# Optimization experiments

Measured on AMD Instinct MI355X. Metric: run time of the kernel, lower is better.

## Reference

```python
import jax, jax.numpy as jnp
import numpy as np

A = 4   # tree arity
D = 7   # tree depth; total nodes = (A**D - 1)//(A - 1) = 5461
B = 64  # batch size
E = 128 # embedding_dim
H = 128 # encode_dim
V = 50000
N_NODES = (A**D - 1) // (A - 1)


def setup_inputs() -> dict:
    key = jax.random.key(0)
    ks = jax.random.split(key, 9)
    tokens = jax.random.randint(ks[0], (N_NODES, B), 0, V, dtype=jnp.int64)
    emb = jax.random.normal(ks[1], (V, E), dtype=jnp.float32) * 0.05
    sent_w = jax.random.normal(ks[2], (H, H), dtype=jnp.float32) * 0.05
    sent_b = jax.random.normal(ks[3], (1, H), dtype=jnp.float32) * 0.05
    ctx_w = jax.random.normal(ks[4], (H, 1), dtype=jnp.float32) * 0.05
    w_ih = jax.random.normal(ks[5], (3 * H, E), dtype=jnp.float32) * 0.05
    w_hh = jax.random.normal(ks[6], (3 * H, H), dtype=jnp.float32) * 0.05
    b_ih = jax.random.normal(ks[7], (3 * H,), dtype=jnp.float32) * 0.05
    b_hh = jax.random.normal(ks[8], (3 * H,), dtype=jnp.float32) * 0.05
    return {"tokens": tokens, "emb": emb, "sent_w": sent_w, "sent_b": sent_b,
            "ctx_w": ctx_w, "w_ih": w_ih, "w_hh": w_hh, "b_ih": b_ih, "b_hh": b_hh}


def _gru_step(x, h, w_ih, w_hh, b_ih, b_hh):
    # x: [n, B, E], h: [n, B, H] -> new hidden [n, B, H]. PyTorch gate order r,z,n.
    gi = jnp.einsum('nbe,ge->nbg', x, w_ih) + b_ih   # [n, B, 3H]
    gh = jnp.einsum('nbh,gh->nbg', h, w_hh) + b_hh
    ir, iz, in_ = jnp.split(gi, 3, axis=-1)
    hr, hz, hn_ = jnp.split(gh, 3, axis=-1)
    r = jax.nn.sigmoid(ir + hr)
    z = jax.nn.sigmoid(iz + hz)
    n = jnp.tanh(in_ + r * hn_)
    return (1.0 - z) * n + z * h


def reference(tokens, emb, sent_w, sent_b, ctx_w, w_ih, w_hh, b_ih, b_hh):
    # Bottom-up over tree levels (level-order storage): level d occupies
    # tokens[(A**d-1)//(A-1) : ... + A**d]. Each node position covers the whole batch.
    hs = None       # hiddens of the level below: [A**(d+1), B, H]
    out_max = None  # running elementwise max over all node hiddens (node_list max)
    for d in range(D - 1, -1, -1):
        n = A ** d
        off = (A ** d - 1) // (A - 1)
        tok = tokens[off:off + n]          # [n, B]
        x = emb[tok]                       # [n, B, E]
        if hs is None:
            h0 = jnp.zeros((n, B, H), dtype=emb.dtype)  # leaves: no children
        else:
            ch = hs.reshape(n, A, B, H)    # children hiddens per parent
            # attention: tanh(ch @ W + b), tanh(. @ ctx), softmax over children
            u = jnp.tanh(jnp.einsum('nabh,hk->nabk', ch, sent_w) + sent_b)
            s = jnp.tanh(jnp.einsum('nabk,k->nab', u, ctx_w[:, 0]))  # [n, A, B]
            alpha = jax.nn.softmax(s, axis=1)                        # over A children
            h0 = jnp.einsum('nabh,nab->nbh', ch, alpha)              # weighted sum
        hn = _gru_step(x, h0, w_ih, w_hh, b_ih, b_hh)                # [n, B, H]
        lvl_max = hn.max(axis=0)                                     # [B, H]
        out_max = lvl_max if out_max is None else jnp.maximum(out_max, lvl_max)
        hs = hn
    return out_max  # [B, H]
```

## Files before the change

kernel.cpp:

```cpp
#include <hip/hip_runtime.h>
#include <cstdint>
#include <cstddef>


typedef short  bf16x8 __attribute__((ext_vector_type(8)));
typedef float  f32x4  __attribute__((ext_vector_type(4)));

#define WS_ACC    0u
#define WS_WIH    1048576u
#define WS_WHH    (WS_WIH + 98304u)
#define WS_SWT    (WS_WHH + 98304u)
#define WS_EMBB   (WS_SWT + 32768u)
#define WS_HLEAF  (WS_EMBB + 12800000u)
#define WS_HA     (WS_HLEAF + 12800000u)
#define WS_HB     (WS_HA + 4194304u)

__device__ __forceinline__ float sigm(float x)   { return 1.0f / (1.0f + __expf(-x)); }
__device__ __forceinline__ float tanhf_(float x) { return 1.0f - 2.0f / (1.0f + __expf(2.0f * x)); }

__device__ __forceinline__ unsigned short f2b(float f) {
  unsigned u = __float_as_uint(f);
  u += 0x7fffu + ((u >> 16) & 1u);
  return (unsigned short)(u >> 16);
}
__device__ __forceinline__ float b2f(unsigned short s) {
  return __uint_as_float(((unsigned)s) << 16);
}

__device__ __forceinline__ unsigned fenc(float f) {
  unsigned u = __float_as_uint(f);
  return (u & 0x80000000u) ? ~u : (u | 0x80000000u);
}
__device__ __forceinline__ float fdec(unsigned e) {
  unsigned u = (e & 0x80000000u) ? (e & 0x7fffffffu) : ~e;
  return __uint_as_float(u);
}

__device__ __forceinline__ f32x4 mfma16(bf16x8 a, bf16x8 b, f32x4 c) {
  return __builtin_amdgcn_mfma_f32_16x16x32_bf16(a, b, c, 0, 0, 0);
}

__global__ __launch_bounds__(256) void decode_out(const unsigned* __restrict__ acc,
                                                  float* __restrict__ out) {
  int i = blockIdx.x * 256 + threadIdx.x;
  unsigned m = 0u;
  for (int s = 0; s < 32; ++s) m = max(m, acc[s * 8192 + i]);
  out[i] = fdec(m);
}

__global__ __launch_bounds__(256) void prep_all(const float* __restrict__ emb,
                                                const float* __restrict__ wih,
                                                const float* __restrict__ whh,
                                                const float* __restrict__ sw,
                                                unsigned short* __restrict__ embb,
                                                unsigned short* __restrict__ wihb,
                                                unsigned short* __restrict__ whhb,
                                                unsigned short* __restrict__ swtb,
                                                unsigned* __restrict__ acc) {
  size_t idx = (size_t)blockIdx.x * 256 + threadIdx.x;
  if (idx < 1600000u) {
    float4 v = *(const float4*)(emb + idx * 4);
    ushort4 o; o.x = f2b(v.x); o.y = f2b(v.y); o.z = f2b(v.z); o.w = f2b(v.w);
    *(ushort4*)(embb + idx * 4) = o;
  } else if (idx < 1714688u) {
    int i = (int)(idx - 1600000u);
    if (i < 49152)       wihb[i] = f2b(wih[i]);
    else if (i < 98304)  whhb[i - 49152] = f2b(whh[i - 49152]);
    else { int j = i - 98304; int k = j >> 7, h = j & 127; swtb[j] = f2b(sw[h * 128 + k]); }
  } else {
    acc[idx - 1714688u] = 0u;
  }
}

__global__ __launch_bounds__(512, 2) void prep_hleaf(
    const unsigned short* __restrict__ embb,
    const unsigned short* __restrict__ wih,
    const float*          __restrict__ b_ih,
    const float*          __restrict__ b_hh,
    unsigned short*       __restrict__ H)
{
  __shared__ unsigned short lds[64 * 128];
  __shared__ unsigned short hvb[64 * 128];
  const int t = threadIdx.x;
  const int base = blockIdx.x * 64;

#pragma unroll
  for (int i = 0; i < 2; ++i) {
    int g = t + 512 * i;
    int m = g >> 4, c = g & 15;
    int v = base + m; if (v > 49999) v = 49999;
    uint4 vv = *(const uint4*)(embb + (size_t)v * 128 + c * 8);
    *(uint4*)(lds + m * 128 + ((c ^ (m & 15)) << 3)) = vv;
  }

  const int w = __builtin_amdgcn_readfirstlane(t >> 6);
  const int lane = t & 63, l = lane & 15, q = lane >> 4;
  const int j = w * 16 + l;

  bf16x8 Br[4], Bz[4], Bn[4];
#pragma unroll
  for (int ks = 0; ks < 4; ++ks) {
    const int ko = ks * 32 + q * 8;
    Br[ks] = *(const bf16x8*)(wih + (size_t)j * 128 + ko);
    Bz[ks] = *(const bf16x8*)(wih + (size_t)(128 + j) * 128 + ko);
    Bn[ks] = *(const bf16x8*)(wih + (size_t)(256 + j) * 128 + ko);
  }
  const float bR = b_ih[j] + b_hh[j];
  const float bZ = b_ih[128 + j] + b_hh[128 + j];
  const float bN = b_ih[256 + j];
  const float bH = b_hh[256 + j];

  f32x4 Cr[4] = {{0,0,0,0},{0,0,0,0},{0,0,0,0},{0,0,0,0}};
  f32x4 Cz[4] = {{0,0,0,0},{0,0,0,0},{0,0,0,0},{0,0,0,0}};
  f32x4 Cn[4] = {{0,0,0,0},{0,0,0,0},{0,0,0,0},{0,0,0,0}};
  __syncthreads();

#pragma unroll
  for (int ks = 0; ks < 4; ++ks) {
    bf16x8 A[4];
#pragma unroll
    for (int mt = 0; mt < 4; ++mt) {
      int m = mt * 16 + l, c = ks * 4 + q;
      A[mt] = *(const bf16x8*)(lds + m * 128 + (((c ^ l) & 15) << 3));
    }
#pragma unroll
    for (int mt = 0; mt < 4; ++mt) {
      Cr[mt] = mfma16(A[mt], Br[ks], Cr[mt]);
      Cz[mt] = mfma16(A[mt], Bz[ks], Cz[mt]);
      Cn[mt] = mfma16(A[mt], Bn[ks], Cn[mt]);
    }
  }

#pragma unroll
  for (int mt = 0; mt < 4; ++mt)
#pragma unroll
    for (int e = 0; e < 4; ++e) {
      int b = mt * 16 + q * 4 + e;
      float r  = sigm(Cr[mt][e] + bR);
      float z  = sigm(Cz[mt][e] + bZ);
      float nv = tanhf_(Cn[mt][e] + bN + r * bH);
      float hv = (1.0f - z) * nv;
      hvb[b * 128 + (j ^ (q << 4))] = f2b(hv);
    }
  __syncthreads();

#pragma unroll
  for (int i = 0; i < 2; ++i) {
    int g = t + 512 * i;
    int b = g >> 4, c8 = (g & 15) * 8;
    int qq = (b >> 2) & 3;
    if (base + b < 50000) {
      uint4 v = *(const uint4*)(hvb + b * 128 + (c8 ^ (qq << 4)));
      *(uint4*)(H + (size_t)(base + b) * 128 + c8) = v;
    }
  }
}

template <bool LEAF>
__global__ __launch_bounds__(512, 4) void attn_gru(
    const unsigned short* __restrict__ hch,
    const int*            __restrict__ tokc,
    const unsigned short* __restrict__ hleaf,
    const unsigned short* __restrict__ swt,
    const float*          __restrict__ sb,
    const float*          __restrict__ ctx,
    const int*            __restrict__ tok,
    const unsigned short* __restrict__ embb,
    const unsigned short* __restrict__ wih,
    const unsigned short* __restrict__ whh,
    const float*          __restrict__ b_ih,
    const float*          __restrict__ b_hh,
    unsigned short*       __restrict__ hout,
    unsigned*             __restrict__ acc)
{
  __shared__ unsigned short chs[128 * 128];
  __shared__ float spart[4][128];
  __shared__ float alf[128];
  unsigned short* const atile = chs;
  unsigned short* const hvb   = chs + 8192;

  const int p2 = blockIdx.x;
  const int p = p2 >> 1, half = p2 & 1;
  const int t = threadIdx.x;

  const int sm = t >> 4, sc = t & 15;
  const int* tp = tok + p * 64 + half * 32;
  uint4 px = *(const uint4*)(embb + (size_t)tp[sm] * 128 + sc * 8);

  if constexpr (LEAF) {
    const int* tokp = tokc + p * 256;
#pragma unroll
    for (int i = 0; i < 4; ++i) {
      int g = t + 512 * i, m = g >> 4, c = g & 15;
      int bg = (m >> 5) * 64 + half * 32 + (m & 31);
      uint4 v = *(const uint4*)(hleaf + (size_t)tokp[bg] * 128 + c * 8);
      *(uint4*)(chs + m * 128 + ((c ^ (m & 15)) << 3)) = v;
    }
  } else {
#pragma unroll
    for (int i = 0; i < 4; ++i) {
      int g = t + 512 * i, m = g >> 4, c = g & 15;
      int bg = (m >> 5) * 64 + half * 32 + (m & 31);
      uint4 v = *(const uint4*)(hch + ((size_t)p * 256 + bg) * 128 + c * 8);
      *(uint4*)(chs + m * 128 + ((c ^ (m & 15)) << 3)) = v;
    }
  }

  const int w = __builtin_amdgcn_readfirstlane(t >> 6);
  const int wm = w >> 2, wn = w & 3;
  const int lane = t & 63, l = lane & 15, q = lane >> 4;
  const int j = w * 16 + l;

  bf16x8 Bs[2][4];
#pragma unroll
  for (int nt = 0; nt < 2; ++nt)
#pragma unroll
    for (int ks = 0; ks < 4; ++ks)
      Bs[nt][ks] = *(const bf16x8*)(swt + (size_t)(wn * 32 + nt * 16 + l) * 128 + ks * 32 + q * 8);

  f32x4 Cu[4][2] = {};
  __syncthreads();

#pragma unroll
  for (int ks = 0; ks < 4; ++ks) {
#pragma unroll
    for (int mt = 0; mt < 4; ++mt) {
      int m = wm * 64 + mt * 16 + l;
      int c = ks * 4 + q;
      bf16x8 A = *(const bf16x8*)(chs + m * 128 + (((c ^ (m & 15)) & 15) << 3));
      Cu[mt][0] = mfma16(A, Bs[0][ks], Cu[mt][0]);
      Cu[mt][1] = mfma16(A, Bs[1][ks], Cu[mt][1]);
    }
  }

  const float sb0 = sb[wn * 32 + l],  sb1 = sb[wn * 32 + 16 + l];
  const float cx0 = ctx[wn * 32 + l], cx1 = ctx[wn * 32 + 16 + l];
#pragma unroll
  for (int mt = 0; mt < 4; ++mt) {
    float pe[4];
#pragma unroll
    for (int e = 0; e < 4; ++e)
      pe[e] = tanhf_(Cu[mt][0][e] + sb0) * cx0 + tanhf_(Cu[mt][1][e] + sb1) * cx1;
#pragma unroll
    for (int mask = 1; mask < 16; mask <<= 1)
#pragma unroll
      for (int e = 0; e < 4; ++e)
        pe[e] += __shfl_xor(pe[e], mask, 16);
    if (l == 0) {
      int r = wm * 64 + mt * 16 + q * 4;
#pragma unroll
      for (int e = 0; e < 4; ++e) spart[wn][r + e] = pe[e];
    }
  }
  __syncthreads();

  if (t < 32) {
    float sv[4];
#pragma unroll
    for (int a = 0; a < 4; ++a) {
      int r = a * 32 + t;
      sv[a] = tanhf_(spart[0][r] + spart[1][r] + spart[2][r] + spart[3][r]);
    }
    float m = fmaxf(fmaxf(sv[0], sv[1]), fmaxf(sv[2], sv[3]));
    float e0 = __expf(sv[0] - m), e1 = __expf(sv[1] - m);
    float e2 = __expf(sv[2] - m), e3 = __expf(sv[3] - m);
    float inv = 1.0f / (e0 + e1 + e2 + e3);
    alf[t] = e0 * inv; alf[32 + t] = e1 * inv; alf[64 + t] = e2 * inv; alf[96 + t] = e3 * inv;
  }
  __syncthreads();

  float o[8] = {0, 0, 0, 0, 0, 0, 0, 0};
  {
    int rb = t >> 4, c = t & 15;
#pragma unroll
    for (int a = 0; a < 4; ++a) {
      int m = a * 32 + rb;
      const unsigned short* rp = chs + m * 128 + ((c ^ (m & 15)) << 3);
      float al = alf[m];
#pragma unroll
      for (int k = 0; k < 8; ++k) o[k] += al * b2f(rp[k]);
    }
  }

  float mxv[8];
  if constexpr (LEAF) {
    const int jj = t & 127, cc = jj >> 3;
#pragma unroll
    for (int e = 0; e < 8; ++e) mxv[e] = -1e30f;
#pragma unroll
    for (int a = 0; a < 4; ++a)
#pragma unroll
      for (int e = 0; e < 8; ++e) {
        int rb = (t >> 7) + 4 * e, m = a * 32 + rb;
        float v = b2f(chs[m * 128 + (((cc ^ (m & 15)) & 15) << 3) + (jj & 7)]);
        mxv[e] = fmaxf(mxv[e], v);
      }
  }
  __syncthreads();

  *(uint4*)(atile + sm * 256 + ((sc ^ (sm & 15)) << 3)) = px;
  {
    int rb = t >> 4, c = t & 15;
    ushort4 ha, hb;
    ha.x = f2b(o[0]); ha.y = f2b(o[1]); ha.z = f2b(o[2]); ha.w = f2b(o[3]);
    hb.x = f2b(o[4]); hb.y = f2b(o[5]); hb.z = f2b(o[6]); hb.w = f2b(o[7]);
    unsigned short* dst = atile + rb * 256 + ((16 | ((c ^ (rb & 15)) & 15)) << 3);
    *(ushort4*)dst = ha;
    *(ushort4*)(dst + 4) = hb;
  }

  const unsigned short* wI = wih + (size_t)j * 128 + q * 8;
  const unsigned short* wH = whh + (size_t)j * 128 + q * 8;
  const float bR = b_ih[j] + b_hh[j];
  const float bZ = b_ih[128 + j] + b_hh[128 + j];
  const float bN = b_ih[256 + j];
  const float bH = b_hh[256 + j];
  __syncthreads();

  f32x4 Cr[2] = {{0,0,0,0},{0,0,0,0}};
  f32x4 Cz[2] = {{0,0,0,0},{0,0,0,0}};
  f32x4 Cn[2] = {{0,0,0,0},{0,0,0,0}};
  f32x4 Ch[2] = {{0,0,0,0},{0,0,0,0}};

  bf16x8 b0 = *(const bf16x8*)(wI);
  bf16x8 b1 = *(const bf16x8*)(wI + 128 * 128);
  bf16x8 b2 = *(const bf16x8*)(wI + 256 * 128);

#pragma unroll
  for (int ks = 0; ks < 8; ++ks) {
    bf16x8 c0 = b0, c1 = b1, c2 = b2;
    if (ks + 1 < 8) {
      const unsigned short* base = (ks + 1 >= 4) ? wH : wI;
      const int ko = ((ks + 1) & 3) * 32;
      b0 = *(const bf16x8*)(base + ko);
      b1 = *(const bf16x8*)(base + 128 * 128 + ko);
      b2 = *(const bf16x8*)(base + 256 * 128 + ko);
    }
#pragma unroll
    for (int mt = 0; mt < 2; ++mt) {
      int m = mt * 16 + l;
      int c = ks * 4 + q;
      bf16x8 Amt = *(const bf16x8*)(atile + m * 256 + (((c & 16) | ((c ^ l) & 15)) << 3));
      Cr[mt] = mfma16(Amt, c0, Cr[mt]);
      Cz[mt] = mfma16(Amt, c1, Cz[mt]);
      if (ks < 4) Cn[mt] = mfma16(Amt, c2, Cn[mt]);
      else        Ch[mt] = mfma16(Amt, c2, Ch[mt]);
    }
  }

  float mx[2][4];
#pragma unroll
  for (int mt = 0; mt < 2; ++mt) {
#pragma unroll
    for (int e = 0; e < 4; ++e) {
      const int b = mt * 16 + q * 4 + e;
      float r  = sigm(Cr[mt][e] + bR);
      float z  = sigm(Cz[mt][e] + bZ);
      float nv = tanhf_(Cn[mt][e] + bN + r * (Ch[mt][e] + bH));
      int c16 = j >> 3;
      float hp = b2f(atile[b * 256 + ((16 | ((c16 ^ (b & 15)) & 15)) << 3) + (j & 7)]);
      float hv = (1.0f - z) * nv + z * hp;
      hvb[b * 128 + (j ^ (q << 4))] = f2b(hv);
      mx[mt][e] = hv;
    }
  }
  __syncthreads();

  {
    int qq = (sm >> 2) & 3;
    uint4 v = *(const uint4*)(hvb + sm * 128 + ((sc * 8) ^ (qq << 4)));
    *(uint4*)(hout + ((size_t)p * 64 + half * 32 + sm) * 128 + sc * 8) = v;
  }

  unsigned* accs = acc + (p2 & 31) * 8192;
#pragma unroll
  for (int mt = 0; mt < 2; ++mt)
#pragma unroll
    for (int e = 0; e < 4; ++e) {
      const int bg = half * 32 + mt * 16 + q * 4 + e;
      atomicMax(accs + bg * 128 + j, fenc(mx[mt][e]));
    }
  if constexpr (LEAF) {
#pragma unroll
    for (int e = 0; e < 8; ++e)
      atomicMax(accs + half * 4096 + t + 512 * e, fenc(mxv[e]));
  }
}

extern "C" void kernel_launch(void* const* d_in, const int* in_sizes, int n_in,
                              void* d_out, int out_size, void* d_ws, size_t ws_size,
                              hipStream_t stream) {
  const int*   tokens = (const int*)d_in[0];
  const float* emb    = (const float*)d_in[1];
  const float* sent_w = (const float*)d_in[2];
  const float* sent_b = (const float*)d_in[3];
  const float* ctx_w  = (const float*)d_in[4];
  const float* w_ih   = (const float*)d_in[5];
  const float* w_hh   = (const float*)d_in[6];
  const float* b_ih   = (const float*)d_in[7];
  const float* b_hh   = (const float*)d_in[8];

  char* ws = (char*)d_ws;
  unsigned*       acc  = (unsigned*)(ws + WS_ACC);
  unsigned short* wihb = (unsigned short*)(ws + WS_WIH);
  unsigned short* whhb = (unsigned short*)(ws + WS_WHH);
  unsigned short* swtb = (unsigned short*)(ws + WS_SWT);
  unsigned short* embb = (unsigned short*)(ws + WS_EMBB);
  unsigned short* hlf  = (unsigned short*)(ws + WS_HLEAF);
  unsigned short* hA   = (unsigned short*)(ws + WS_HA);
  unsigned short* hB   = (unsigned short*)(ws + WS_HB);

  hipLaunchKernelGGL(prep_all, dim3(7722), dim3(256), 0, stream,
                     emb, w_ih, w_hh, sent_w, embb, wihb, whhb, swtb, acc);
  hipLaunchKernelGGL(prep_hleaf, dim3(782), dim3(512), 0, stream,
                     embb, wihb, b_ih, b_hh, hlf);

  static const int offs[7] = {0, 1, 5, 21, 85, 341, 1365};
  const int* tok6 = tokens + (size_t)1365 * 64;

  for (int d = 5; d >= 0; --d) {
    int n = 1 << (2 * d);
    unsigned short* hout  = (d & 1) ? hB : hA;
    unsigned short* child = (d & 1) ? hA : hB;
    if (d == 5) {
      hipLaunchKernelGGL((attn_gru<true>), dim3(2 * n), dim3(512), 0, stream,
                         (const unsigned short*)nullptr, tok6, hlf,
                         swtb, sent_b, ctx_w,
                         tokens + (size_t)offs[5] * 64, embb, wihb, whhb,
                         b_ih, b_hh, hout, acc);
    } else {
      hipLaunchKernelGGL((attn_gru<false>), dim3(2 * n), dim3(512), 0, stream,
                         child, (const int*)nullptr, (const unsigned short*)nullptr,
                         swtb, sent_b, ctx_w,
                         tokens + (size_t)offs[d] * 64, embb, wihb, whhb,
                         b_ih, b_hh, hout, acc);
    }
  }
  hipLaunchKernelGGL(decode_out, dim3(32), dim3(256), 0, stream, acc, (float*)d_out);
}
```

Baseline: 309.4 us.

## Make attn_gru persistent over multiple parents with register prefetch of next tile

Result: slower. 475.5 us (+53.7%).

```diff
diff --git a/kernel.cpp b/kernel.cpp
--- a/kernel.cpp
+++ b/kernel.cpp
@@ -171,40 +171,23 @@
     const float*          __restrict__ b_ih,
     const float*          __restrict__ b_hh,
     unsigned short*       __restrict__ hout,
-    unsigned*             __restrict__ acc)
+    unsigned*             __restrict__ acc,
+    int nPar, int npp)
 {
   __shared__ unsigned short chs[128 * 128];
+  __shared__ unsigned short hvb[32 * 128];
   __shared__ float spart[4][128];
   __shared__ float alf[128];
   unsigned short* const atile = chs;
-  unsigned short* const hvb   = chs + 8192;
-
-  const int p2 = blockIdx.x;
-  const int p = p2 >> 1, half = p2 & 1;
+
+  const int G = gridDim.x >> 1;
+  const int half = (blockIdx.x >= G) ? 1 : 0;
+  const int pBeg = (blockIdx.x - (half ? G : 0)) * npp;
+  const int pEnd = min(nPar, pBeg + npp);
+  if (pBeg >= nPar) return;
+
   const int t = threadIdx.x;
-
   const int sm = t >> 4, sc = t & 15;
-  const int* tp = tok + p * 64 + half * 32;
-  uint4 px = *(const uint4*)(embb + (size_t)tp[sm] * 128 + sc * 8);
-
-  if constexpr (LEAF) {
-    const int* tokp = tokc + p * 256;
-#pragma unroll
-    for (int i = 0; i < 4; ++i) {
-      int g = t + 512 * i, m = g >> 4, c = g & 15;
-      int bg = (m >> 5) * 64 + half * 32 + (m & 31);
-      uint4 v = *(const uint4*)(hleaf + (size_t)tokp[bg] * 128 + c * 8);
-      *(uint4*)(chs + m * 128 + ((c ^ (m & 15)) << 3)) = v;
-    }
-  } else {
-#pragma unroll
-    for (int i = 0; i < 4; ++i) {
-      int g = t + 512 * i, m = g >> 4, c = g & 15;
-      int bg = (m >> 5) * 64 + half * 32 + (m & 31);
-      uint4 v = *(const uint4*)(hch + ((size_t)p * 256 + bg) * 128 + c * 8);
-      *(uint4*)(chs + m * 128 + ((c ^ (m & 15)) << 3)) = v;
-    }
-  }
 
   const int w = __builtin_amdgcn_readfirstlane(t >> 6);
   const int wm = w >> 2, wn = w & 3;
@@ -218,96 +201,8 @@
     for (int ks = 0; ks < 4; ++ks)
       Bs[nt][ks] = *(const bf16x8*)(swt + (size_t)(wn * 32 + nt * 16 + l) * 128 + ks * 32 + q * 8);
 
-  f32x4 Cu[4][2] = {};
-  __syncthreads();
-
-#pragma unroll
-  for (int ks = 0; ks < 4; ++ks) {
-#pragma unroll
-    for (int mt = 0; mt < 4; ++mt) {
-      int m = wm * 64 + mt * 16 + l;
-      int c = ks * 4 + q;
-      bf16x8 A = *(const bf16x8*)(chs + m * 128 + (((c ^ (m & 15)) & 15) << 3));
-      Cu[mt][0] = mfma16(A, Bs[0][ks], Cu[mt][0]);
-      Cu[mt][1] = mfma16(A, Bs[1][ks], Cu[mt][1]);
-    }
-  }
-
   const float sb0 = sb[wn * 32 + l],  sb1 = sb[wn * 32 + 16 + l];
   const float cx0 = ctx[wn * 32 + l], cx1 = ctx[wn * 32 + 16 + l];
-#pragma unroll
-  for (int mt = 0; mt < 4; ++mt) {
-    float pe[4];
-#pragma unroll
-    for (int e = 0; e < 4; ++e)
-      pe[e] = tanhf_(Cu[mt][0][e] + sb0) * cx0 + tanhf_(Cu[mt][1][e] + sb1) * cx1;
-#pragma unroll
-    for (int mask = 1; mask < 16; mask <<= 1)
-#pragma unroll
-      for (int e = 0; e < 4; ++e)
-        pe[e] += __shfl_xor(pe[e], mask, 16);
-    if (l == 0) {
-      int r = wm * 64 + mt * 16 + q * 4;
-#pragma unroll
-      for (int e = 0; e < 4; ++e) spart[wn][r + e] = pe[e];
-    }
-  }
-  __syncthreads();
-
-  if (t < 32) {
-    float sv[4];
-#pragma unroll
-    for (int a = 0; a < 4; ++a) {
-      int r = a * 32 + t;
-      sv[a] = tanhf_(spart[0][r] + spart[1][r] + spart[2][r] + spart[3][r]);
-    }
-    float m = fmaxf(fmaxf(sv[0], sv[1]), fmaxf(sv[2], sv[3]));
-    float e0 = __expf(sv[0] - m), e1 = __expf(sv[1] - m);
-    float e2 = __expf(sv[2] - m), e3 = __expf(sv[3] - m);
-    float inv = 1.0f / (e0 + e1 + e2 + e3);
-    alf[t] = e0 * inv; alf[32 + t] = e1 * inv; alf[64 + t] = e2 * inv; alf[96 + t] = e3 * inv;
-  }
-  __syncthreads();
-
-  float o[8] = {0, 0, 0, 0, 0, 0, 0, 0};
-  {
-    int rb = t >> 4, c = t & 15;
-#pragma unroll
-    for (int a = 0; a < 4; ++a) {
-      int m = a * 32 + rb;
-      const unsigned short* rp = chs + m * 128 + ((c ^ (m & 15)) << 3);
-      float al = alf[m];
-#pragma unroll
-      for (int k = 0; k < 8; ++k) o[k] += al * b2f(rp[k]);
-    }
-  }
-
-  float mxv[8];
-  if constexpr (LEAF) {
-    const int jj = t & 127, cc = jj >> 3;
-#pragma unroll
-    for (int e = 0; e < 8; ++e) mxv[e] = -1e30f;
-#pragma unroll
-    for (int a = 0; a < 4; ++a)
-#pragma unroll
-      for (int e = 0; e < 8; ++e) {
-        int rb = (t >> 7) + 4 * e, m = a * 32 + rb;
-        float v = b2f(chs[m * 128 + (((cc ^ (m & 15)) & 15) << 3) + (jj & 7)]);
-        mxv[e] = fmaxf(mxv[e], v);
-      }
-  }
-  __syncthreads();
-
-  *(uint4*)(atile + sm * 256 + ((sc ^ (sm & 15)) << 3)) = px;
-  {
-    int rb = t >> 4, c = t & 15;
-    ushort4 ha, hb;
-    ha.x = f2b(o[0]); ha.y = f2b(o[1]); ha.z = f2b(o[2]); ha.w = f2b(o[3]);
-    hb.x = f2b(o[4]); hb.y = f2b(o[5]); hb.z = f2b(o[6]); hb.w = f2b(o[7]);
-    unsigned short* dst = atile + rb * 256 + ((16 | ((c ^ (rb & 15)) & 15)) << 3);
-    *(ushort4*)dst = ha;
-    *(ushort4*)(dst + 4) = hb;
-  }
 
   const unsigned short* wI = wih + (size_t)j * 128 + q * 8;
   const unsigned short* wH = whh + (size_t)j * 128 + q * 8;
@@ -315,64 +210,196 @@
   const float bZ = b_ih[128 + j] + b_hh[128 + j];
   const float bN = b_ih[256 + j];
   const float bH = b_hh[256 + j];
-  __syncthreads();
-
-  f32x4 Cr[2] = {{0,0,0,0},{0,0,0,0}};
-  f32x4 Cz[2] = {{0,0,0,0},{0,0,0,0}};
-  f32x4 Cn[2] = {{0,0,0,0},{0,0,0,0}};
-  f32x4 Ch[2] = {{0,0,0,0},{0,0,0,0}};
-
-  bf16x8 b0 = *(const bf16x8*)(wI);
-  bf16x8 b1 = *(const bf16x8*)(wI + 128 * 128);
-  bf16x8 b2 = *(const bf16x8*)(wI + 256 * 128);
-
-#pragma unroll
-  for (int ks = 0; ks < 8; ++ks) {
-    bf16x8 c0 = b0, c1 = b1, c2 = b2;
-    if (ks + 1 < 8) {
-      const unsigned short* base = (ks + 1 >= 4) ? wH : wI;
-      const int ko = ((ks + 1) & 3) * 32;
-      b0 = *(const bf16x8*)(base + ko);
-      b1 = *(const bf16x8*)(base + 128 * 128 + ko);
-      b2 = *(const bf16x8*)(base + 256 * 128 + ko);
-    }
+
+  float mx[2][4];
+#pragma unroll
+  for (int mt = 0; mt < 2; ++mt)
+#pragma unroll
+    for (int e = 0; e < 4; ++e) mx[mt][e] = -1e30f;
+  float mxv[8];
+#pragma unroll
+  for (int e = 0; e < 8; ++e) mxv[e] = -1e30f;
+
+  uint4 pc0, pc1, pc2, pc3, px;
+  {
+    const int p = pBeg;
+#pragma unroll
+    for (int i = 0; i < 4; ++i) {
+      int g = t + 512 * i, m = g >> 4, c = g & 15;
+      int bg = (m >> 5) * 64 + half * 32 + (m & 31);
+      uint4 v;
+      if constexpr (LEAF) v = *(const uint4*)(hleaf + (size_t)(tokc + p * 256)[bg] * 128 + c * 8);
+      else                v = *(const uint4*)(hch + ((size_t)p * 256 + bg) * 128 + c * 8);
+      if (i == 0) pc0 = v; else if (i == 1) pc1 = v; else if (i == 2) pc2 = v; else pc3 = v;
+    }
+    px = *(const uint4*)(embb + (size_t)(tok + p * 64 + half * 32)[sm] * 128 + sc * 8);
+  }
+
+  for (int p = pBeg; p < pEnd; ++p) {
+#pragma unroll
+    for (int i = 0; i < 4; ++i) {
+      int g = t + 512 * i, m = g >> 4, c = g & 15;
+      uint4 v = (i == 0) ? pc0 : (i == 1) ? pc1 : (i == 2) ? pc2 : pc3;
+      *(uint4*)(chs + m * 128 + ((c ^ (m & 15)) << 3)) = v;
+    }
+    const uint4 xcur = px;
+    __syncthreads();
+
+    f32x4 Cu[4][2] = {};
+#pragma unroll
+    for (int ks = 0; ks < 4; ++ks) {
+#pragma unroll
+      for (int mt = 0; mt < 4; ++mt) {
+        int m = wm * 64 + mt * 16 + l;
+        int c = ks * 4 + q;
+        bf16x8 A = *(const bf16x8*)(chs + m * 128 + (((c ^ (m & 15)) & 15) << 3));
+        Cu[mt][0] = mfma16(A, Bs[0][ks], Cu[mt][0]);
+        Cu[mt][1] = mfma16(A, Bs[1][ks], Cu[mt][1]);
+      }
+    }
+
+#pragma unroll
+    for (int mt = 0; mt < 4; ++mt) {
+      float pe[4];
+#pragma unroll
+      for (int e = 0; e < 4; ++e)
+        pe[e] = tanhf_(Cu[mt][0][e] + sb0) * cx0 + tanhf_(Cu[mt][1][e] + sb1) * cx1;
+#pragma unroll
+      for (int mask = 1; mask < 16; mask <<= 1)
+#pragma unroll
+        for (int e = 0; e < 4; ++e)
+          pe[e] += __shfl_xor(pe[e], mask, 16);
+      if (l == 0) {
+        int r = wm * 64 + mt * 16 + q * 4;
+#pragma unroll
+        for (int e = 0; e < 4; ++e) spart[wn][r + e] = pe[e];
+      }
+    }
+    __syncthreads();
+
+    if (t < 32) {
+      float sv[4];
+#pragma unroll
+      for (int a = 0; a < 4; ++a) {
+        int r = a * 32 + t;
+        sv[a] = tanhf_(spart[0][r] + spart[1][r] + spart[2][r] + spart[3][r]);
+      }
+      float m = fmaxf(fmaxf(sv[0], sv[1]), fmaxf(sv[2], sv[3]));
+      float e0 = __expf(sv[0] - m), e1 = __expf(sv[1] - m);
+      float e2 = __expf(sv[2] - m), e3 = __expf(sv[3] - m);
+      float inv = 1.0f / (e0 + e1 + e2 + e3);
+      alf[t] = e0 * inv; alf[32 + t] = e1 * inv; alf[64 + t] = e2 * inv; alf[96 + t] = e3 * inv;
+    }
+    __syncthreads();
+
+    float o[8] = {0, 0, 0, 0, 0, 0, 0, 0};
+    {
+      int rb = t >> 4, c = t & 15;
+#pragma unroll
+      for (int a = 0; a < 4; ++a) {
+        int m = a * 32 + rb;
+        const unsigned short* rp = chs + m * 128 + ((c ^ (m & 15)) << 3);
+        float al = alf[m];
+#pragma unroll
+        for (int k = 0; k < 8; ++k) o[k] += al * b2f(rp[k]);
+      }
+    }
+
+    if constexpr (LEAF) {
+      const int jj = t & 127, cc = jj >> 3;
+#pragma unroll
+      for (int a = 0; a < 4; ++a)
+#pragma unroll
+        for (int e = 0; e < 8; ++e) {
+          int rb = (t >> 7) + 4 * e, m = a * 32 + rb;
+          float v = b2f(chs[m * 128 + (((cc ^ (m & 15)) & 15) << 3) + (jj & 7)]);
+          mxv[e] = fmaxf(mxv[e], v);
+        }
+    }
+    __syncthreads();
+
+    *(uint4*)(atile + sm * 256 + ((sc ^ (sm & 15)) << 3)) = xcur;
+    {
+      int rb = t >> 4, c = t & 15;
+      ushort4 ha, hb;
+      ha.x = f2b(o[0]); ha.y = f2b(o[1]); ha.z = f2b(o[2]); ha.w = f2b(o[3]);
+      hb.x = f2b(o[4]); hb.y = f2b(o[5]); hb.z = f2b(o[6]); hb.w = f2b(o[7]);
+      unsigned short* dst = atile + rb * 256 + ((16 | ((c ^ (rb & 15)) & 15)) << 3);
+      *(ushort4*)dst = ha;
+      *(ushort4*)(dst + 4) = hb;
+    }
+
+    if (p + 1 < pEnd) {
+      const int pn = p + 1;
+#pragma unroll
+      for (int i = 0; i < 4; ++i) {
+        int g = t + 512 * i, m = g >> 4, c = g & 15;
+        int bg = (m >> 5) * 64 + half * 32 + (m & 31);
+        uint4 v;
+        if constexpr (LEAF) v = *(const uint4*)(hleaf + (size_t)(tokc + pn * 256)[bg] * 128 + c * 8);
+        else                v = *(const uint4*)(hch + ((size_t)pn * 256 + bg) * 128 + c * 8);
+        if (i == 0) pc0 = v; else if (i == 1) pc1 = v; else if (i == 2) pc2 = v; else pc3 = v;
+      }
+      px = *(const uint4*)(embb + (size_t)(tok + pn * 64 + half * 32)[sm] * 128 + sc * 8);
+    }
+    __syncthreads();
+
+    f32x4 Cr[2] = {{0,0,0,0},{0,0,0,0}};
+    f32x4 Cz[2] = {{0,0,0,0},{0,0,0,0}};
+    f32x4 Cn[2] = {{0,0,0,0},{0,0,0,0}};
+    f32x4 Ch[2] = {{0,0,0,0},{0,0,0,0}};
+
+    bf16x8 b0 = *(const bf16x8*)(wI);
+    bf16x8 b1 = *(const bf16x8*)(wI + 128 * 128);
+    bf16x8 b2 = *(const bf16x8*)(wI + 256 * 128);
+
+#pragma unroll
+    for (int ks = 0; ks < 8; ++ks) {
+      bf16x8 c0 = b0, c1 = b1, c2 = b2;
+      if (ks + 1 < 8) {
+        const unsigned short* base = (ks + 1 >= 4) ? wH : wI;
+        const int ko = ((ks + 1) & 3) * 32;
+        b0 = *(const bf16x8*)(base + ko);
+        b1 = *(const bf16x8*)(base + 128 * 128 + ko);
+        b2 = *(const bf16x8*)(base + 256 * 128 + ko);
+      }
+#pragma unroll
+      for (int mt = 0; mt < 2; ++mt) {
+        int m = mt * 16 + l;
+        int c = ks * 4 + q;
+        bf16x8 Amt = *(const bf16x8*)(atile + m * 256 + (((c & 16) | ((c ^ l) & 15)) << 3));
+        Cr[mt] = mfma16(Amt, c0, Cr[mt]);
+        Cz[mt] = mfma16(Amt, c1, Cz[mt]);
+        if (ks < 4) Cn[mt] = mfma16(Amt, c2, Cn[mt]);
+        else        Ch[mt] = mfma16(Amt, c2, Ch[mt]);
+      }
+    }
+
 #pragma unroll
     for (int mt = 0; mt < 2; ++mt) {
-      int m = mt * 16 + l;
-      int c = ks * 4 + q;
-      bf16x8 Amt = *(const bf16x8*)(atile + m * 256 + (((c & 16) | ((c ^ l) & 15)) << 3));
-      Cr[mt] = mfma16(Amt, c0, Cr[mt]);
-      Cz[mt] = mfma16(Amt, c1, Cz[mt]);
-      if (ks < 4) Cn[mt] = mfma16(Amt, c2, Cn[mt]);
-      else        Ch[mt] = mfma16(Amt, c2, Ch[mt]);
-    }
-  }
-
-  float mx[2][4];
-#pragma unroll
-  for (int mt = 0; mt < 2; ++mt) {
-#pragma unroll
-    for (int e = 0; e < 4; ++e) {
-      const int b = mt * 16 + q * 4 + e;
-      float r  = sigm(Cr[mt][e] + bR);
-      float z  = sigm(Cz[mt][e] + bZ);
-      float nv = tanhf_(Cn[mt][e] + bN + r * (Ch[mt][e] + bH));
-      int c16 = j >> 3;
-      float hp = b2f(atile[b * 256 + ((16 | ((c16 ^ (b & 15)) & 15)) << 3) + (j & 7)]);
-      float hv = (1.0f - z) * nv + z * hp;
-      hvb[b * 128 + (j ^ (q << 4))] = f2b(hv);
-      mx[mt][e] = hv;
-    }
-  }
-  __syncthreads();
-
-  {
-    int qq = (sm >> 2) & 3;
-    uint4 v = *(const uint4*)(hvb + sm * 128 + ((sc * 8) ^ (qq << 4)));
-    *(uint4*)(hout + ((size_t)p * 64 + half * 32 + sm) * 128 + sc * 8) = v;
-  }
-
-  unsigned* accs = acc + (p2 & 31) * 8192;
+#pragma unroll
+      for (int e = 0; e < 4; ++e) {
+        const int b = mt * 16 + q * 4 + e;
+        float r  = sigm(Cr[mt][e] + bR);
+        float z  = sigm(Cz[mt][e] + bZ);
+        float nv = tanhf_(Cn[mt][e] + bN + r * (Ch[mt][e] + bH));
+        int c16 = j >> 3;
+        float hp = b2f(atile[b * 256 + ((16 | ((c16 ^ (b & 15)) & 15)) << 3) + (j & 7)]);
+        float hv = (1.0f - z) * nv + z * hp;
+        hvb[b * 128 + (j ^ (q << 4))] = f2b(hv);
+        mx[mt][e] = fmaxf(mx[mt][e], hv);
+      }
+    }
+    __syncthreads();
+
+    {
+      int qq = (sm >> 2) & 3;
+      uint4 v = *(const uint4*)(hvb + sm * 128 + ((sc * 8) ^ (qq << 4)));
+      *(uint4*)(hout + ((size_t)p * 64 + half * 32 + sm) * 128 + sc * 8) = v;
+    }
+  }
+
+  unsigned* accs = acc + (blockIdx.x & 31) * 8192;
 #pragma unroll
   for (int mt = 0; mt < 2; ++mt)
 #pragma unroll
@@ -420,20 +447,22 @@
 
   for (int d = 5; d >= 0; --d) {
     int n = 1 << (2 * d);
+    int G   = n < 256 ? n : 256;
+    int npp = (n + G - 1) / G;
     unsigned short* hout  = (d & 1) ? hB : hA;
     unsigned short* child = (d & 1) ? hA : hB;
     if (d == 5) {
-      hipLaunchKernelGGL((attn_gru<true>), dim3(2 * n), dim3(512), 0, stream,
+      hipLaunchKernelGGL((attn_gru<true>), dim3(2 * G), dim3(512), 0, stream,
                          (const unsigned short*)nullptr, tok6, hlf,
                          swtb, sent_b, ctx_w,
                          tokens + (size_t)offs[5] * 64, embb, wihb, whhb,
-                         b_ih, b_hh, hout, acc);
+                         b_ih, b_hh, hout, acc, n, npp);
     } else {
-      hipLaunchKernelGGL((attn_gru<false>), dim3(2 * n), dim3(512), 0, stream,
+      hipLaunchKernelGGL((attn_gru<false>), dim3(2 * G), dim3(512), 0, stream,
                          child, (const int*)nullptr, (const unsigned short*)nullptr,
                          swtb, sent_b, ctx_w,
                          tokens + (size_t)offs[d] * 64, embb, wihb, whhb,
-                         b_ih, b_hh, hout, acc);
+                         b_ih, b_hh, hout, acc, n, npp);
     }
   }
   hipLaunchKernelGGL(decode_out, dim3(32), dim3(256), 0, stream, acc, (float*)d_out);
```
